# Kernel tuning notes

Measured on AMD Instinct MI355X. Metric: run time of the kernel, lower is better.

Reference implementation:

```python
import jax, jax.numpy as jnp
import numpy as np

B, S, D, H = 2, 2048, 1024, 16
DH = D // H
ROPE_BASE = 10000.0


def apply_rope(x):
    # x: [B, H, S, DH]; rotate-half RoPE, base 10000
    half = DH // 2
    inv_freq = 1.0 / (ROPE_BASE ** (jnp.arange(half, dtype=jnp.float32) / half))
    ang = jnp.arange(S, dtype=jnp.float32)[:, None] * inv_freq[None, :]  # [S, half]
    cos = jnp.cos(ang)[None, None]  # [1,1,S,half]
    sin = jnp.sin(ang)[None, None]
    x1, x2 = x[..., :half], x[..., half:]
    return jnp.concatenate([x1 * cos - x2 * sin, x1 * sin + x2 * cos], axis=-1)


def setup_inputs() -> dict:
    key = jax.random.key(0)
    ks = jax.random.split(key, 9)
    w = lambda k: jax.random.normal(k, (D, D), dtype=jnp.float32) * 0.02
    return {
        "x": jax.random.normal(ks[0], (B, S, D), dtype=jnp.float32),
        "Wq": w(ks[1]), "bq": jnp.zeros((D,), jnp.float32),
        "Wk": w(ks[2]), "bk": jnp.zeros((D,), jnp.float32),
        "Wv": w(ks[3]), "bv": jnp.zeros((D,), jnp.float32),
        "Wo": w(ks[4]), "bo": jnp.zeros((D,), jnp.float32),
    }


def reference(x, Wq, bq, Wk, bk, Wv, bv, Wo, bo):
    # projections (W stored as [in, out])
    q = x @ Wq + bq
    k = x @ Wk + bk
    v = x @ Wv + bv
    # [B, S, D] -> [B, H, S, DH]
    to_heads = lambda t: t.reshape(B, S, H, DH).transpose(0, 2, 1, 3)
    q, k, v = to_heads(q), to_heads(k), to_heads(v)
    q = apply_rope(q)
    k = apply_rope(k)
    scores = jnp.einsum("bhqd,bhkd->bhqk", q, k) / jnp.sqrt(jnp.float32(DH))
    causal = jnp.tril(jnp.ones((S, S), dtype=bool))  # [S, S]
    scores = jnp.where(causal[None, None], scores, -jnp.inf)
    probs = jax.nn.softmax(scores, axis=-1)
    ctx = jnp.einsum("bhqk,bhkd->bhqd", probs, v)
    ctx = ctx.transpose(0, 2, 1, 3).reshape(B, S, D)  # concat heads
    return ctx @ Wo + bo
```

## Files before the change

### kernel.cpp

```cpp
#include <hip/hip_runtime.h>
#include <hip/hip_bf16.h>

#define B_  2
#define S_  2048
#define D_  1024
#define H_  16
#define DH_ 64

typedef __attribute__((ext_vector_type(8))) short bf16x8;
typedef __attribute__((ext_vector_type(4))) float f32x4;

__device__ __forceinline__ short f2bf(float f) {
  unsigned int u; __builtin_memcpy(&u, &f, 4);
  u = (u + 0x7FFFu + ((u >> 16) & 1u)) >> 16;
  return (short)u;
}
__device__ __forceinline__ unsigned cvtpk(float a, float b) {
  unsigned r;
  asm("v_cvt_pk_bf16_f32 %0, %1, %2" : "=v"(r) : "v"(a), "v"(b));
  return r;
}

#define GLOAD_LDS16(gp, lp) \
  __builtin_amdgcn_global_load_lds((const __attribute__((address_space(1))) void*)(gp), \
                                   (__attribute__((address_space(3))) void*)(lp), 16, 0, 0)

#define MFMA16(a, b, c) __builtin_amdgcn_mfma_f32_16x16x32_bf16(a, b, c, 0, 0, 0)

union U8 { unsigned u[4]; bf16x8 v; };

__global__ __launch_bounds__(256) void k_cvt(const float* __restrict__ in,
                                             short* __restrict__ out, int n4) {
  int i = blockIdx.x * 256 + threadIdx.x;
  if (i >= n4) return;
  float4 v = ((const float4*)in)[i];
  short4 o; o.x = f2bf(v.x); o.y = f2bf(v.y); o.z = f2bf(v.z); o.w = f2bf(v.w);
  *(short4*)(out + (size_t)i * 4) = o;
}

__global__ __launch_bounds__(256) void k_transpose4(const float* __restrict__ W0,
                                                    const float* __restrict__ W1,
                                                    const float* __restrict__ W2,
                                                    const float* __restrict__ W3,
                                                    short* __restrict__ WtBase) {
  __shared__ float tile[32][33];
  const float* W = (blockIdx.z == 0) ? W0 : (blockIdx.z == 1) ? W1 :
                   (blockIdx.z == 2) ? W2 : W3;
  short* Wt = WtBase + (size_t)blockIdx.z * D_ * D_;
  int tx = threadIdx.x, ty = threadIdx.y;
  int bx = blockIdx.x * 32, by = blockIdx.y * 32;
  #pragma unroll
  for (int i = 0; i < 32; i += 8)
    tile[ty + i][tx] = W[(size_t)(by + ty + i) * D_ + bx + tx];
  __syncthreads();
  #pragma unroll
  for (int i = 0; i < 32; i += 8)
    Wt[(size_t)(bx + ty + i) * D_ + by + tx] = f2bf(tile[tx][ty + i]);
}

__global__ __launch_bounds__(256) void k_rope_table(float* __restrict__ cosT,
                                                    float* __restrict__ sinT) {
  int i = blockIdx.x * 256 + threadIdx.x;
  int s = i >> 5, d = i & 31;
  float invf = exp2f(-(float)d * (13.287712379549449f / 32.0f));
  float ang = (float)s * invf;
  cosT[i] = cosf(ang);
  sinT[i] = sinf(ang);
}

__global__ __launch_bounds__(256) void k_gemm_qkv(const short* __restrict__ A,
                                                  const short* __restrict__ Bt,
                                                  const float* __restrict__ bq,
                                                  const float* __restrict__ bk,
                                                  const float* __restrict__ bv,
                                                  const float* __restrict__ cosT,
                                                  const float* __restrict__ sinT,
                                                  short* __restrict__ qb,
                                                  short* __restrict__ kb,
                                                  short* __restrict__ vb) {
  const int K = 1024;
  __shared__ __align__(16) short lA[128 * 32];
  __shared__ __align__(16) short lB[128 * 32];
  const int tid = threadIdx.x;
  const int wid = tid >> 6, lane = tid & 63;
  const int brow = blockIdx.y * 128, bcol = blockIdx.x * 128;
  const int wr = wid >> 1, wc = wid & 1;
  const int g = lane >> 4, c15 = lane & 15;
  const int sr = lane >> 2, scol = (lane & 3) * 8;
  f32x4 acc[4][4] = {};

  for (int kt = 0; kt < K; kt += 32) {
    __syncthreads();
    #pragma unroll
    for (int ch = 0; ch < 2; ++ch) {
      const short* ga = A + (size_t)(brow + ch * 64 + wid * 16 + sr) * K + kt + scol;
      const short* gb = Bt + (size_t)(bcol + ch * 64 + wid * 16 + sr) * K + kt + scol;
      GLOAD_LDS16(ga, &lA[(ch * 64 + wid * 16) * 32]);
      GLOAD_LDS16(gb, &lB[(ch * 64 + wid * 16) * 32]);
    }
    __syncthreads();
    bf16x8 af[4], bfr[4];
    #pragma unroll
    for (int mi = 0; mi < 4; ++mi)
      af[mi] = *(const bf16x8*)&lA[(wr * 64 + mi * 16 + c15) * 32 + g * 8];
    #pragma unroll
    for (int ni = 0; ni < 4; ++ni)
      bfr[ni] = *(const bf16x8*)&lB[(wc * 64 + ni * 16 + c15) * 32 + g * 8];
    #pragma unroll
    for (int mi = 0; mi < 4; ++mi)
      #pragma unroll
      for (int ni = 0; ni < 4; ++ni)
        acc[mi][ni] = MFMA16(af[mi], bfr[ni], acc[mi][ni]);
  }

  const int seg = bcol >> 10;
  const float* bp = (seg == 0) ? bq : (seg == 1) ? bk : bv;
  short* dst = (seg == 0) ? qb : (seg == 1) ? kb : vb;
  const float alpha = (seg == 0) ? 0.18033688f : 1.0f;
  const bool rope = (seg < 2);
  #pragma unroll
  for (int mi = 0; mi < 4; ++mi) {
    #pragma unroll
    for (int ni = 0; ni < 2; ++ni) {
      int col  = bcol + wc * 64 + ni * 16 + c15;
      int lcol = col & 1023;
      int d    = col & 63;
      float b1 = bp[lcol], b2 = bp[lcol + 32];
      #pragma unroll
      for (int r = 0; r < 4; ++r) {
        int row = brow + wr * 64 + mi * 16 + g * 4 + r;
        float x1 = (acc[mi][ni][r]     + b1) * alpha;
        float x2 = (acc[mi][ni + 2][r] + b2) * alpha;
        float o1 = x1, o2 = x2;
        if (rope) {
          int s = row & (S_ - 1);
          float co = cosT[s * 32 + d], si = sinT[s * 32 + d];
          o1 = x1 * co - x2 * si;
          o2 = x1 * si + x2 * co;
        }
        dst[(size_t)row * 1024 + lcol]      = f2bf(o1);
        dst[(size_t)row * 1024 + lcol + 32] = f2bf(o2);
      }
    }
  }
}

__global__ __launch_bounds__(256) void k_gemm(const short* __restrict__ A,
                                              const short* __restrict__ Bt,
                                              const float* __restrict__ bias,
                                              float* __restrict__ out,
                                              int M, int N, int K) {
  __shared__ __align__(16) short lA[128 * 32];
  __shared__ __align__(16) short lB[128 * 32];
  const int tid = threadIdx.x;
  const int wid = tid >> 6, lane = tid & 63;
  const int brow = blockIdx.y * 128, bcol = blockIdx.x * 128;
  const int wr = wid >> 1, wc = wid & 1;
  const int g = lane >> 4, c15 = lane & 15;
  const int sr = lane >> 2, scol = (lane & 3) * 8;
  f32x4 acc[4][4] = {};

  for (int kt = 0; kt < K; kt += 32) {
    __syncthreads();
    #pragma unroll
    for (int ch = 0; ch < 2; ++ch) {
      const short* ga = A + (size_t)(brow + ch * 64 + wid * 16 + sr) * K + kt + scol;
      const short* gb = Bt + (size_t)(bcol + ch * 64 + wid * 16 + sr) * K + kt + scol;
      GLOAD_LDS16(ga, &lA[(ch * 64 + wid * 16) * 32]);
      GLOAD_LDS16(gb, &lB[(ch * 64 + wid * 16) * 32]);
    }
    __syncthreads();
    bf16x8 af[4], bfr[4];
    #pragma unroll
    for (int mi = 0; mi < 4; ++mi)
      af[mi] = *(const bf16x8*)&lA[(wr * 64 + mi * 16 + c15) * 32 + g * 8];
    #pragma unroll
    for (int ni = 0; ni < 4; ++ni)
      bfr[ni] = *(const bf16x8*)&lB[(wc * 64 + ni * 16 + c15) * 32 + g * 8];
    #pragma unroll
    for (int mi = 0; mi < 4; ++mi)
      #pragma unroll
      for (int ni = 0; ni < 4; ++ni)
        acc[mi][ni] = MFMA16(af[mi], bfr[ni], acc[mi][ni]);
  }

  #pragma unroll
  for (int mi = 0; mi < 4; ++mi) {
    #pragma unroll
    for (int ni = 0; ni < 4; ++ni) {
      int col = bcol + wc * 64 + ni * 16 + c15;
      float bv = bias[col];
      #pragma unroll
      for (int r = 0; r < 4; ++r) {
        int row = brow + wr * 64 + mi * 16 + g * 4 + r;
        out[(size_t)row * N + col] = acc[mi][ni][r] + bv;
      }
    }
  }
}

__device__ __forceinline__ void softmax_g(f32x4 (&s)[4], float& m, float& l,
                                          f32x4 (&o)[4], int g) {
  float pm = -1e30f;
  #pragma unroll
  for (int n = 0; n < 4; ++n)
    #pragma unroll
    for (int r = 0; r < 4; ++r) pm = fmaxf(pm, s[n][r]);
  pm = fmaxf(pm, __shfl_xor(pm, 16));
  pm = fmaxf(pm, __shfl_xor(pm, 32));
  if (!__all(pm <= m + 8.0f)) {
    float nm = fmaxf(m, pm);
    float corr = exp2f(m - nm);
    m = nm; l *= corr;
    float cf[4];
    #pragma unroll
    for (int r = 0; r < 4; ++r) cf[r] = __shfl(corr, g * 4 + r);
    #pragma unroll
    for (int dblk = 0; dblk < 4; ++dblk)
      #pragma unroll
      for (int r = 0; r < 4; ++r) o[dblk][r] *= cf[r];
  }
  float rs = 0.0f;
  #pragma unroll
  for (int n = 0; n < 4; ++n)
    #pragma unroll
    for (int r = 0; r < 4; ++r) {
      float p = exp2f(s[n][r] - m);
      s[n][r] = p; rs += p;
    }
  rs += __shfl_xor(rs, 16);
  rs += __shfl_xor(rs, 32);
  l += rs;
}

__device__ __forceinline__ void build_pa(const f32x4 (&s)[4], U8 (&pa)[2],
                                         int g, int c15) {
  unsigned pk[4][2];
  #pragma unroll
  for (int n = 0; n < 4; ++n) {
    pk[n][0] = cvtpk(s[n][0], s[n][1]);
    pk[n][1] = cvtpk(s[n][2], s[n][3]);
  }
  #pragma unroll
  for (int kh = 0; kh < 2; ++kh) {
    #pragma unroll
    for (int widx = 0; widx < 4; ++widx) {
      int src = (2 * (g & 1) + (widx >> 1)) * 16 + c15;
      unsigned lo = __shfl(pk[2 * kh][widx & 1], src);
      unsigned hi = __shfl(pk[2 * kh + 1][widx & 1], src);
      pa[kh].u[widx] = (g & 2) ? hi : lo;
    }
  }
}

__global__ __launch_bounds__(512) void k_flash(const short* __restrict__ Qb,
                                               const short* __restrict__ Kb,
                                               const short* __restrict__ Vb,
                                               short* __restrict__ Ctx,
                                               float* __restrict__ pO,
                                               float* __restrict__ pML) {
  __shared__ __align__(16) short Vt[2][64][72];
  __shared__ __align__(16) short Kl[2][4096];
  const int bid = blockIdx.x;
  const int sched = bid >> 5, bh = bid & 31;
  const unsigned char QTs[22] = {9,8,15,15,7,14,14,6,13,13,12,12,5,11,11,10,10,4,3,2,1,0};
  const unsigned char MDs[22] = {0,0,1, 2, 0,1, 2, 0,1, 2, 1, 2, 0,1, 2, 1, 2, 0,0,0,0,0};
  const int qt = QTs[sched], md = MDs[sched];
  int t0, t1;
  if (md == 0)      { t0 = 0;      t1 = 2 * qt + 1; }
  else if (md == 1) { t0 = 0;      t1 = qt; }
  else              { t0 = qt + 1; t1 = 2 * qt + 1; }
  const bool split = (md != 0);
  const int sid = bh * 12 + (qt - 10) * 2 + (md == 2 ? 1 : 0);
  const int b   = bh >> 4, h = bh & 15;
  const int tid = threadIdx.x, w = tid >> 6, lane = tid & 63;
  const int g   = lane >> 4, c15 = lane & 15;
  const int qg0 = qt * 128 + w * 16;
  const int qabs = qg0 + c15;

  const short* qp = Qb + ((size_t)(b * S_ + qabs)) * D_ + h * DH_ + g * 8;
  bf16x8 qf0 = *(const bf16x8*)qp;
  bf16x8 qf1 = *(const bf16x8*)(qp + 32);

  const int vkv = lane;
  const int vd0 = w * 8;
  const int vcol = vkv ^ ((w >> 1) << 3);
  const short* vrow = Vb + (size_t)b * S_ * D_ + h * DH_ + vd0;

  const short* kbase = Kb + (size_t)b * S_ * D_ + h * DH_;
  const int kidx = w * 64 + lane;
  const int kkv = kidx >> 3, kdb = (kidx & 7) ^ (kkv & 7);

  f32x4 o[4] = {};
  float m = -1e30f, l = 0.0f;

  {
    const short* kb0 = kbase + (size_t)(t0 * 64) * D_;
    GLOAD_LDS16(kb0 + (size_t)kkv * D_ + kdb * 8, &Kl[t0 & 1][kidx * 8]);
    const short* vp = vrow + (size_t)(t0 * 64 + vkv) * D_;
    bf16x8 a = *(const bf16x8*)vp;
    #pragma unroll
    for (int j = 0; j < 8; ++j) Vt[t0 & 1][vd0 + j][vcol] = a[j];
  }
  __syncthreads();

  for (int t = t0; t <= t1; ++t) {
    const int kv0 = t * 64;
    bf16x8 nv;
    if (t + 1 <= t1) {
      const short* kb2 = kbase + (size_t)(kv0 + 64) * D_;
      GLOAD_LDS16(kb2 + (size_t)kkv * D_ + kdb * 8, &Kl[(t + 1) & 1][kidx * 8]);
      nv = *(const bf16x8*)(vrow + (size_t)(kv0 + 64 + vkv) * D_);
    }
    if (kv0 <= qg0 + 15) {
      const short* ks = &Kl[t & 1][0];
      f32x4 s[4] = {};
      __builtin_amdgcn_s_setprio(1);
      #pragma unroll
      for (int n = 0; n < 4; ++n) {
        int krow = (n * 16 + c15) * 64;
        bf16x8 k0 = *(const bf16x8*)&ks[krow + ((g ^ (c15 & 7)) * 8)];
        bf16x8 k1 = *(const bf16x8*)&ks[krow + (((g + 4) ^ (c15 & 7)) * 8)];
        s[n] = MFMA16(k0, qf0, s[n]);
        s[n] = MFMA16(k1, qf1, s[n]);
      }
      __builtin_amdgcn_s_setprio(0);
      if (kv0 + 63 > qg0) {
        #pragma unroll
        for (int n = 0; n < 4; ++n)
          #pragma unroll
          for (int r = 0; r < 4; ++r)
            if (kv0 + n * 16 + g * 4 + r > qabs) s[n][r] = -1e30f;
      }
      softmax_g(s, m, l, o, g);
      U8 pa[2];
      build_pa(s, pa, g, c15);
      __builtin_amdgcn_s_setprio(1);
      #pragma unroll
      for (int kh = 0; kh < 2; ++kh)
        #pragma unroll
        for (int dblk = 0; dblk < 4; ++dblk) {
          bf16x8 vbf = *(const bf16x8*)&Vt[t & 1][dblk * 16 + c15][kh * 32 + ((g ^ dblk) * 8)];
          o[dblk] = MFMA16(pa[kh].v, vbf, o[dblk]);
        }
      __builtin_amdgcn_s_setprio(0);
    }
    if (t + 1 <= t1) {
      #pragma unroll
      for (int j = 0; j < 8; ++j) Vt[(t + 1) & 1][vd0 + j][vcol] = nv[j];
    }
    __syncthreads();
  }

  if (!split) {
    float linv = 1.0f / l;
    float lf[4];
    #pragma unroll
    for (int r = 0; r < 4; ++r) lf[r] = __shfl(linv, g * 4 + r);
    #pragma unroll
    for (int dblk = 0; dblk < 4; ++dblk)
      #pragma unroll
      for (int r = 0; r < 4; ++r) {
        int q = qg0 + g * 4 + r;
        Ctx[((size_t)(b * S_ + q)) * D_ + h * DH_ + dblk * 16 + c15] = f2bf(o[dblk][r] * lf[r]);
      }
  } else {
    float* po = pO + ((size_t)sid * 128 + w * 16) * 64;
    #pragma unroll
    for (int dblk = 0; dblk < 4; ++dblk)
      #pragma unroll
      for (int r = 0; r < 4; ++r)
        po[(g * 4 + r) * 64 + dblk * 16 + c15] = o[dblk][r];
    if (lane < 16) {
      pML[(size_t)sid * 256 + w * 16 + lane]       = m;
      pML[(size_t)sid * 256 + 128 + w * 16 + lane] = l;
    }
  }
}

__global__ __launch_bounds__(256) void k_combine(const float* __restrict__ pO,
                                                 const float* __restrict__ pML,
                                                 short* __restrict__ Ctx) {
  const int p = blockIdx.x;
  const int qt = 10 + (p >> 5), bh = p & 31;
  const int b = bh >> 4, h = bh & 15;
  const int sidA = bh * 12 + (qt - 10) * 2;
  const int sidB = sidA + 1;
  const int row = threadIdx.x >> 1;
  const int d0 = (threadIdx.x & 1) * 32;
  float mA = pML[(size_t)sidA * 256 + row], lA = pML[(size_t)sidA * 256 + 128 + row];
  float mB = pML[(size_t)sidB * 256 + row], lB = pML[(size_t)sidB * 256 + 128 + row];
  float M = fmaxf(mA, mB);
  float wA = exp2f(mA - M), wB = exp2f(mB - M);
  float inv = 1.0f / (lA * wA + lB * wB);
  const float* oA = pO + ((size_t)sidA * 128 + row) * 64 + d0;
  const float* oB = pO + ((size_t)sidB * 128 + row) * 64 + d0;
  short* cp = Ctx + ((size_t)(b * S_ + qt * 128 + row)) * D_ + h * DH_ + d0;
  #pragma unroll
  for (int i = 0; i < 32; i += 4) {
    float4 a = *(const float4*)(oA + i);
    float4 c = *(const float4*)(oB + i);
    cp[i + 0] = f2bf((a.x * wA + c.x * wB) * inv);
    cp[i + 1] = f2bf((a.y * wA + c.y * wB) * inv);
    cp[i + 2] = f2bf((a.z * wA + c.z * wB) * inv);
    cp[i + 3] = f2bf((a.w * wA + c.w * wB) * inv);
  }
}

extern "C" void kernel_launch(void* const* d_in, const int* in_sizes, int n_in,
                              void* d_out, int out_size, void* d_ws, size_t ws_size,
                              hipStream_t stream) {
  (void)in_sizes; (void)n_in; (void)out_size; (void)ws_size;
  const float* x  = (const float*)d_in[0];
  const float* Wq = (const float*)d_in[1];
  const float* bq = (const float*)d_in[2];
  const float* Wk = (const float*)d_in[3];
  const float* bk = (const float*)d_in[4];
  const float* Wv = (const float*)d_in[5];
  const float* bv = (const float*)d_in[6];
  const float* Wo = (const float*)d_in[7];
  const float* bo = (const float*)d_in[8];
  float* out = (float*)d_out;
  char* ws = (char*)d_ws;

  const size_t MS = (size_t)B_ * S_;
  short* xb  = (short*)(ws);
  short* wqT = (short*)(ws + (size_t)8 * 1024 * 1024);
  short* wkT = wqT + (size_t)D_ * D_;
  short* wvT = wkT + (size_t)D_ * D_;
  short* woT = wvT + (size_t)D_ * D_;
  short* qb  = (short*)(ws + (size_t)16 * 1024 * 1024);
  short* kb  = qb + MS * D_;
  short* vb  = kb + MS * D_;
  short* ctx = vb + MS * D_;
  float* cosT = (float*)(ws + (size_t)48 * 1024 * 1024);
  float* sinT = cosT + (size_t)S_ * 32;
  float* pO  = (float*)(ws);
  float* pML = (float*)(ws + (size_t)48 * 1024 * 1024 + 512 * 1024);

  k_cvt<<<dim3((unsigned)(MS * D_ / 4 / 256)), 256, 0, stream>>>(x, xb, (int)(MS * D_ / 4));
  k_transpose4<<<dim3(32, 32, 4), dim3(32, 8), 0, stream>>>(Wq, Wk, Wv, Wo, wqT);
  k_rope_table<<<dim3(S_ * 32 / 256), 256, 0, stream>>>(cosT, sinT);
  k_gemm_qkv<<<dim3(24, 32), 256, 0, stream>>>(xb, wqT, bq, bk, bv, cosT, sinT, qb, kb, vb);
  k_flash<<<dim3(22 * 32), 512, 0, stream>>>(qb, kb, vb, ctx, pO, pML);
  k_combine<<<dim3(6 * 32), 256, 0, stream>>>(pO, pML, ctx);
  k_gemm<<<dim3(8, 32), 256, 0, stream>>>(ctx, woT, bo, out, 4096, 1024, 1024);
}
```

Baseline: 142.7 us.

## Switch flash attention to 32x32 MFMA with 4 waves, swizzle GEMM blocks, fuse prep kernels

The flash attention kernel now uses 32x32x16 bf16 MFMA tiles with 4 waves of 32 query rows each instead of 8 waves of 16 rows. K loads are staged through registers instead of direct-to-LDS loads, the P matrix is rearranged with permlane32 swaps instead of shuffles, and a raw barrier is used. Separately, both GEMMs remap block indices so that neighbouring blocks share tiles in L2, and the bf16 conversion and RoPE table kernels are merged into one launch. Fewer waves per block lowers latency hiding, and register pressure from the f32x16 accumulators rises.

Result: faster. 137.2 us (-3.9%).

```diff
diff --git a/kernel.cpp b/kernel.cpp
--- a/kernel.cpp
+++ b/kernel.cpp
@@ -9,6 +9,7 @@
 
 typedef __attribute__((ext_vector_type(8))) short bf16x8;
 typedef __attribute__((ext_vector_type(4))) float f32x4;
+typedef __attribute__((ext_vector_type(16))) float f32x16;
 
 __device__ __forceinline__ short f2bf(float f) {
   unsigned int u; __builtin_memcpy(&u, &f, 4);
@@ -20,22 +21,43 @@
   asm("v_cvt_pk_bf16_f32 %0, %1, %2" : "=v"(r) : "v"(a), "v"(b));
   return r;
 }
+__device__ __forceinline__ void plswap(unsigned &a, unsigned &b) {
+  asm("v_permlane32_swap_b32 %0, %1" : "+v"(a), "+v"(b));
+}
 
 #define GLOAD_LDS16(gp, lp) \
   __builtin_amdgcn_global_load_lds((const __attribute__((address_space(1))) void*)(gp), \
                                    (__attribute__((address_space(3))) void*)(lp), 16, 0, 0)
 
 #define MFMA16(a, b, c) __builtin_amdgcn_mfma_f32_16x16x32_bf16(a, b, c, 0, 0, 0)
+#define MFMA32(a, b, c) __builtin_amdgcn_mfma_f32_32x32x16_bf16(a, b, c, 0, 0, 0)
+
+#define RAW_BARRIER() do {                                   \
+    asm volatile("s_waitcnt lgkmcnt(0)" ::: "memory");       \
+    __builtin_amdgcn_s_barrier();                            \
+    asm volatile("" ::: "memory");                           \
+  } while (0)
 
 union U8 { unsigned u[4]; bf16x8 v; };
 
-__global__ __launch_bounds__(256) void k_cvt(const float* __restrict__ in,
-                                             short* __restrict__ out, int n4) {
-  int i = blockIdx.x * 256 + threadIdx.x;
-  if (i >= n4) return;
-  float4 v = ((const float4*)in)[i];
-  short4 o; o.x = f2bf(v.x); o.y = f2bf(v.y); o.z = f2bf(v.z); o.w = f2bf(v.w);
-  *(short4*)(out + (size_t)i * 4) = o;
+__global__ __launch_bounds__(256) void k_cvt_table(const float* __restrict__ in,
+                                                   short* __restrict__ out,
+                                                   float* __restrict__ cosT,
+                                                   float* __restrict__ sinT) {
+  int bid = blockIdx.x;
+  if (bid < 4096) {
+    int i = bid * 256 + threadIdx.x;
+    float4 v = ((const float4*)in)[i];
+    short4 o; o.x = f2bf(v.x); o.y = f2bf(v.y); o.z = f2bf(v.z); o.w = f2bf(v.w);
+    *(short4*)(out + (size_t)i * 4) = o;
+  } else {
+    int i = (bid - 4096) * 256 + threadIdx.x;
+    int s = i >> 5, d = i & 31;
+    float invf = exp2f(-(float)d * (13.287712379549449f / 32.0f));
+    float ang = (float)s * invf;
+    cosT[i] = cosf(ang);
+    sinT[i] = sinf(ang);
+  }
 }
 
 __global__ __launch_bounds__(256) void k_transpose4(const float* __restrict__ W0,
@@ -58,16 +80,6 @@
     Wt[(size_t)(bx + ty + i) * D_ + by + tx] = f2bf(tile[tx][ty + i]);
 }
 
-__global__ __launch_bounds__(256) void k_rope_table(float* __restrict__ cosT,
-                                                    float* __restrict__ sinT) {
-  int i = blockIdx.x * 256 + threadIdx.x;
-  int s = i >> 5, d = i & 31;
-  float invf = exp2f(-(float)d * (13.287712379549449f / 32.0f));
-  float ang = (float)s * invf;
-  cosT[i] = cosf(ang);
-  sinT[i] = sinf(ang);
-}
-
 __global__ __launch_bounds__(256) void k_gemm_qkv(const short* __restrict__ A,
                                                   const short* __restrict__ Bt,
                                                   const float* __restrict__ bq,
@@ -81,9 +93,12 @@
   const int K = 1024;
   __shared__ __align__(16) short lA[128 * 32];
   __shared__ __align__(16) short lB[128 * 32];
+  const int fid = blockIdx.y * 24 + blockIdx.x;
+  const int swz = (fid & 7) * 96 + (fid >> 3);
+  const int bxs = swz % 24, bys = swz / 24;
   const int tid = threadIdx.x;
   const int wid = tid >> 6, lane = tid & 63;
-  const int brow = blockIdx.y * 128, bcol = blockIdx.x * 128;
+  const int brow = bys * 128, bcol = bxs * 128;
   const int wr = wid >> 1, wc = wid & 1;
   const int g = lane >> 4, c15 = lane & 15;
   const int sr = lane >> 2, scol = (lane & 3) * 8;
@@ -152,9 +167,12 @@
                                               int M, int N, int K) {
   __shared__ __align__(16) short lA[128 * 32];
   __shared__ __align__(16) short lB[128 * 32];
+  const int fid = blockIdx.y * 8 + blockIdx.x;
+  const int swz = (fid & 7) * 32 + (fid >> 3);
+  const int bxs = swz % 8, bys = swz / 8;
   const int tid = threadIdx.x;
   const int wid = tid >> 6, lane = tid & 63;
-  const int brow = blockIdx.y * 128, bcol = blockIdx.x * 128;
+  const int brow = bys * 128, bcol = bxs * 128;
   const int wr = wid >> 1, wc = wid & 1;
   const int g = lane >> 4, c15 = lane & 15;
   const int sr = lane >> 2, scol = (lane & 3) * 8;
@@ -199,61 +217,7 @@
   }
 }
 
-__device__ __forceinline__ void softmax_g(f32x4 (&s)[4], float& m, float& l,
-                                          f32x4 (&o)[4], int g) {
-  float pm = -1e30f;
-  #pragma unroll
-  for (int n = 0; n < 4; ++n)
-    #pragma unroll
-    for (int r = 0; r < 4; ++r) pm = fmaxf(pm, s[n][r]);
-  pm = fmaxf(pm, __shfl_xor(pm, 16));
-  pm = fmaxf(pm, __shfl_xor(pm, 32));
-  if (!__all(pm <= m + 8.0f)) {
-    float nm = fmaxf(m, pm);
-    float corr = exp2f(m - nm);
-    m = nm; l *= corr;
-    float cf[4];
-    #pragma unroll
-    for (int r = 0; r < 4; ++r) cf[r] = __shfl(corr, g * 4 + r);
-    #pragma unroll
-    for (int dblk = 0; dblk < 4; ++dblk)
-      #pragma unroll
-      for (int r = 0; r < 4; ++r) o[dblk][r] *= cf[r];
-  }
-  float rs = 0.0f;
-  #pragma unroll
-  for (int n = 0; n < 4; ++n)
-    #pragma unroll
-    for (int r = 0; r < 4; ++r) {
-      float p = exp2f(s[n][r] - m);
-      s[n][r] = p; rs += p;
-    }
-  rs += __shfl_xor(rs, 16);
-  rs += __shfl_xor(rs, 32);
-  l += rs;
-}
-
-__device__ __forceinline__ void build_pa(const f32x4 (&s)[4], U8 (&pa)[2],
-                                         int g, int c15) {
-  unsigned pk[4][2];
-  #pragma unroll
-  for (int n = 0; n < 4; ++n) {
-    pk[n][0] = cvtpk(s[n][0], s[n][1]);
-    pk[n][1] = cvtpk(s[n][2], s[n][3]);
-  }
-  #pragma unroll
-  for (int kh = 0; kh < 2; ++kh) {
-    #pragma unroll
-    for (int widx = 0; widx < 4; ++widx) {
-      int src = (2 * (g & 1) + (widx >> 1)) * 16 + c15;
-      unsigned lo = __shfl(pk[2 * kh][widx & 1], src);
-      unsigned hi = __shfl(pk[2 * kh + 1][widx & 1], src);
-      pa[kh].u[widx] = (g & 2) ? hi : lo;
-    }
-  }
-}
-
-__global__ __launch_bounds__(512) void k_flash(const short* __restrict__ Qb,
+__global__ __launch_bounds__(256) void k_flash(const short* __restrict__ Qb,
                                                const short* __restrict__ Kb,
                                                const short* __restrict__ Vb,
                                                short* __restrict__ Ctx,
@@ -274,106 +238,162 @@
   const int sid = bh * 12 + (qt - 10) * 2 + (md == 2 ? 1 : 0);
   const int b   = bh >> 4, h = bh & 15;
   const int tid = threadIdx.x, w = tid >> 6, lane = tid & 63;
-  const int g   = lane >> 4, c15 = lane & 15;
-  const int qg0 = qt * 128 + w * 16;
-  const int qabs = qg0 + c15;
-
-  const short* qp = Qb + ((size_t)(b * S_ + qabs)) * D_ + h * DH_ + g * 8;
-  bf16x8 qf0 = *(const bf16x8*)qp;
-  bf16x8 qf1 = *(const bf16x8*)(qp + 32);
+  const int c31 = lane & 31, hi = lane >> 5;
+  const int qg0 = qt * 128 + w * 32;
+  const int qabs = qg0 + c31;
+
+  bf16x8 qf[4];
+  {
+    const short* qp = Qb + ((size_t)(b * S_ + qabs)) * D_ + h * DH_ + hi * 8;
+    #pragma unroll
+    for (int ko = 0; ko < 4; ++ko) qf[ko] = *(const bf16x8*)(qp + ko * 16);
+  }
 
   const int vkv = lane;
-  const int vd0 = w * 8;
-  const int vcol = vkv ^ ((w >> 1) << 3);
+  const int vd0 = w * 16;
+  const int vcol = vkv ^ (w << 3);
   const short* vrow = Vb + (size_t)b * S_ * D_ + h * DH_ + vd0;
 
   const short* kbase = Kb + (size_t)b * S_ * D_ + h * DH_;
-  const int kidx = w * 64 + lane;
-  const int kkv = kidx >> 3, kdb = (kidx & 7) ^ (kkv & 7);
-
-  f32x4 o[4] = {};
+  const int kidx0 = w * 128 + lane;
+  const int kkv0 = kidx0 >> 3, kdb0 = (kidx0 & 7) ^ (kkv0 & 7);
+  const int kidx1 = kidx0 + 64;
+  const int kkv1 = kidx1 >> 3, kdb1 = (kidx1 & 7) ^ (kkv1 & 7);
+
+  f32x16 o0 = {}, o1 = {};
   float m = -1e30f, l = 0.0f;
+
+  bf16x8 kc0, kc1, vc0, vc1;
 
   {
     const short* kb0 = kbase + (size_t)(t0 * 64) * D_;
-    GLOAD_LDS16(kb0 + (size_t)kkv * D_ + kdb * 8, &Kl[t0 & 1][kidx * 8]);
+    bf16x8 tk0 = *(const bf16x8*)(kb0 + (size_t)kkv0 * D_ + kdb0 * 8);
+    bf16x8 tk1 = *(const bf16x8*)(kb0 + (size_t)kkv1 * D_ + kdb1 * 8);
     const short* vp = vrow + (size_t)(t0 * 64 + vkv) * D_;
-    bf16x8 a = *(const bf16x8*)vp;
-    #pragma unroll
-    for (int j = 0; j < 8; ++j) Vt[t0 & 1][vd0 + j][vcol] = a[j];
-  }
-  __syncthreads();
+    bf16x8 tv0 = *(const bf16x8*)vp;
+    bf16x8 tv1 = *(const bf16x8*)(vp + 8);
+    *(bf16x8*)&Kl[t0 & 1][kidx0 * 8] = tk0;
+    *(bf16x8*)&Kl[t0 & 1][kidx1 * 8] = tk1;
+    #pragma unroll
+    for (int j = 0; j < 8; ++j) Vt[t0 & 1][vd0 + j][vcol] = tv0[j];
+    #pragma unroll
+    for (int j = 0; j < 8; ++j) Vt[t0 & 1][vd0 + 8 + j][vcol] = tv1[j];
+  }
+  RAW_BARRIER();
 
   for (int t = t0; t <= t1; ++t) {
     const int kv0 = t * 64;
-    bf16x8 nv;
     if (t + 1 <= t1) {
-      const short* kb2 = kbase + (size_t)(kv0 + 64) * D_;
-      GLOAD_LDS16(kb2 + (size_t)kkv * D_ + kdb * 8, &Kl[(t + 1) & 1][kidx * 8]);
-      nv = *(const bf16x8*)(vrow + (size_t)(kv0 + 64 + vkv) * D_);
-    }
-    if (kv0 <= qg0 + 15) {
+      const short* kb1 = kbase + (size_t)(kv0 + 64) * D_;
+      kc0 = *(const bf16x8*)(kb1 + (size_t)kkv0 * D_ + kdb0 * 8);
+      kc1 = *(const bf16x8*)(kb1 + (size_t)kkv1 * D_ + kdb1 * 8);
+      const short* vp1 = vrow + (size_t)(kv0 + 64 + vkv) * D_;
+      vc0 = *(const bf16x8*)vp1;
+      vc1 = *(const bf16x8*)(vp1 + 8);
+    }
+    if (kv0 <= qg0 + 31) {
       const short* ks = &Kl[t & 1][0];
-      f32x4 s[4] = {};
+      f32x16 s0 = {}, s1 = {};
       __builtin_amdgcn_s_setprio(1);
       #pragma unroll
-      for (int n = 0; n < 4; ++n) {
-        int krow = (n * 16 + c15) * 64;
-        bf16x8 k0 = *(const bf16x8*)&ks[krow + ((g ^ (c15 & 7)) * 8)];
-        bf16x8 k1 = *(const bf16x8*)&ks[krow + (((g + 4) ^ (c15 & 7)) * 8)];
-        s[n] = MFMA16(k0, qf0, s[n]);
-        s[n] = MFMA16(k1, qf1, s[n]);
+      for (int ko = 0; ko < 4; ++ko) {
+        bf16x8 k0 = *(const bf16x8*)&ks[(c31) * 64 + (((ko * 2 + hi) ^ (c31 & 7)) * 8)];
+        bf16x8 k1 = *(const bf16x8*)&ks[(32 + c31) * 64 + (((ko * 2 + hi) ^ (c31 & 7)) * 8)];
+        s0 = MFMA32(k0, qf[ko], s0);
+        s1 = MFMA32(k1, qf[ko], s1);
       }
       __builtin_amdgcn_s_setprio(0);
       if (kv0 + 63 > qg0) {
         #pragma unroll
-        for (int n = 0; n < 4; ++n)
-          #pragma unroll
-          for (int r = 0; r < 4; ++r)
-            if (kv0 + n * 16 + g * 4 + r > qabs) s[n][r] = -1e30f;
-      }
-      softmax_g(s, m, l, o, g);
-      U8 pa[2];
-      build_pa(s, pa, g, c15);
+        for (int r = 0; r < 16; ++r) {
+          int cr = (r & 3) + 8 * (r >> 2) + 4 * hi;
+          if (kv0 + cr > qabs)      s0[r] = -1e30f;
+          if (kv0 + 32 + cr > qabs) s1[r] = -1e30f;
+        }
+      }
+      float pm = -1e30f;
+      #pragma unroll
+      for (int r = 0; r < 16; ++r) { pm = fmaxf(pm, s0[r]); pm = fmaxf(pm, s1[r]); }
+      pm = fmaxf(pm, __shfl_xor(pm, 32));
+      if (!__all(pm <= m + 8.0f)) {
+        float nm = fmaxf(m, pm);
+        float corr = exp2f(m - nm);
+        m = nm; l *= corr;
+        #pragma unroll
+        for (int r = 0; r < 16; ++r) {
+          float cf = __shfl(corr, (r & 3) + 8 * (r >> 2) + 4 * hi);
+          o0[r] *= cf; o1[r] *= cf;
+        }
+      }
+      float rs = 0.0f;
+      #pragma unroll
+      for (int r = 0; r < 16; ++r) {
+        float p0 = exp2f(s0[r] - m);
+        float p1 = exp2f(s1[r] - m);
+        s0[r] = p0; s1[r] = p1; rs += p0 + p1;
+      }
+      rs += __shfl_xor(rs, 32);
+      l += rs;
+      U8 pa[4];
+      #pragma unroll
+      for (int kb = 0; kb < 2; ++kb) {
+        const f32x16& sv = kb ? s1 : s0;
+        #pragma unroll
+        for (int h2 = 0; h2 < 2; ++h2) {
+          int base = h2 * 8;
+          unsigned a0 = cvtpk(sv[base + 0], sv[base + 1]);
+          unsigned b0 = cvtpk(sv[base + 4], sv[base + 5]);
+          unsigned a1 = cvtpk(sv[base + 2], sv[base + 3]);
+          unsigned b1 = cvtpk(sv[base + 6], sv[base + 7]);
+          plswap(a0, b0); plswap(a1, b1);
+          pa[kb * 2 + h2].u[0] = a0; pa[kb * 2 + h2].u[1] = a1;
+          pa[kb * 2 + h2].u[2] = b0; pa[kb * 2 + h2].u[3] = b1;
+        }
+      }
       __builtin_amdgcn_s_setprio(1);
       #pragma unroll
-      for (int kh = 0; kh < 2; ++kh)
-        #pragma unroll
-        for (int dblk = 0; dblk < 4; ++dblk) {
-          bf16x8 vbf = *(const bf16x8*)&Vt[t & 1][dblk * 16 + c15][kh * 32 + ((g ^ dblk) * 8)];
-          o[dblk] = MFMA16(pa[kh].v, vbf, o[dblk]);
-        }
+      for (int ks = 0; ks < 4; ++ks) {
+        int r0 = c31;
+        int r1 = 32 + c31;
+        bf16x8 v0 = *(const bf16x8*)&Vt[t & 1][r0][(ks * 16 + hi * 8) ^ (((r0 >> 4) & 3) << 3)];
+        bf16x8 v1 = *(const bf16x8*)&Vt[t & 1][r1][(ks * 16 + hi * 8) ^ (((r1 >> 4) & 3) << 3)];
+        o0 = MFMA32(pa[ks].v, v0, o0);
+        o1 = MFMA32(pa[ks].v, v1, o1);
+      }
       __builtin_amdgcn_s_setprio(0);
     }
     if (t + 1 <= t1) {
-      #pragma unroll
-      for (int j = 0; j < 8; ++j) Vt[(t + 1) & 1][vd0 + j][vcol] = nv[j];
-    }
-    __syncthreads();
+      *(bf16x8*)&Kl[(t + 1) & 1][kidx0 * 8] = kc0;
+      *(bf16x8*)&Kl[(t + 1) & 1][kidx1 * 8] = kc1;
+      #pragma unroll
+      for (int j = 0; j < 8; ++j) Vt[(t + 1) & 1][vd0 + j][vcol] = vc0[j];
+      #pragma unroll
+      for (int j = 0; j < 8; ++j) Vt[(t + 1) & 1][vd0 + 8 + j][vcol] = vc1[j];
+      RAW_BARRIER();
+    }
   }
 
   if (!split) {
     float linv = 1.0f / l;
-    float lf[4];
-    #pragma unroll
-    for (int r = 0; r < 4; ++r) lf[r] = __shfl(linv, g * 4 + r);
-    #pragma unroll
-    for (int dblk = 0; dblk < 4; ++dblk)
-      #pragma unroll
-      for (int r = 0; r < 4; ++r) {
-        int q = qg0 + g * 4 + r;
-        Ctx[((size_t)(b * S_ + q)) * D_ + h * DH_ + dblk * 16 + c15] = f2bf(o[dblk][r] * lf[r]);
-      }
+    #pragma unroll
+    for (int r = 0; r < 16; ++r) {
+      int cr = (r & 3) + 8 * (r >> 2) + 4 * hi;
+      float cf = __shfl(linv, cr);
+      short* cp = Ctx + ((size_t)(b * S_ + qg0 + cr)) * D_ + h * DH_ + c31;
+      cp[0]  = f2bf(o0[r] * cf);
+      cp[32] = f2bf(o1[r] * cf);
+    }
   } else {
-    float* po = pO + ((size_t)sid * 128 + w * 16) * 64;
-    #pragma unroll
-    for (int dblk = 0; dblk < 4; ++dblk)
-      #pragma unroll
-      for (int r = 0; r < 4; ++r)
-        po[(g * 4 + r) * 64 + dblk * 16 + c15] = o[dblk][r];
-    if (lane < 16) {
-      pML[(size_t)sid * 256 + w * 16 + lane]       = m;
-      pML[(size_t)sid * 256 + 128 + w * 16 + lane] = l;
+    float* po = pO + ((size_t)sid * 128 + w * 32) * 64;
+    #pragma unroll
+    for (int r = 0; r < 16; ++r) {
+      int cr = (r & 3) + 8 * (r >> 2) + 4 * hi;
+      po[cr * 64 + c31]      = o0[r];
+      po[cr * 64 + 32 + c31] = o1[r];
+    }
+    if (lane < 32) {
+      pML[(size_t)sid * 256 + w * 32 + lane]       = m;
+      pML[(size_t)sid * 256 + 128 + w * 32 + lane] = l;
     }
   }
 }
@@ -438,11 +458,10 @@
   float* pO  = (float*)(ws);
   float* pML = (float*)(ws + (size_t)48 * 1024 * 1024 + 512 * 1024);
 
-  k_cvt<<<dim3((unsigned)(MS * D_ / 4 / 256)), 256, 0, stream>>>(x, xb, (int)(MS * D_ / 4));
+  k_cvt_table<<<dim3(4096 + 256), 256, 0, stream>>>(x, xb, cosT, sinT);
   k_transpose4<<<dim3(32, 32, 4), dim3(32, 8), 0, stream>>>(Wq, Wk, Wv, Wo, wqT);
-  k_rope_table<<<dim3(S_ * 32 / 256), 256, 0, stream>>>(cosT, sinT);
   k_gemm_qkv<<<dim3(24, 32), 256, 0, stream>>>(xb, wqT, bq, bk, bv, cosT, sinT, qb, kb, vb);
-  k_flash<<<dim3(22 * 32), 512, 0, stream>>>(qb, kb, vb, ctx, pO, pML);
+  k_flash<<<dim3(22 * 32), 256, 0, stream>>>(qb, kb, vb, ctx, pO, pML);
   k_combine<<<dim3(6 * 32), 256, 0, stream>>>(pO, pML, ctx);
   k_gemm<<<dim3(8, 32), 256, 0, stream>>>(ctx, woT, bo, out, 4096, 1024, 1024);
 }
```
